# Kernel optimization log

Hardware: AMD Instinct MI355X
Metric: run time of the kernel (lower is better)

The kernel has to match this reference:

```python
import jax, jax.numpy as jnp
import numpy as np

GAMMA = 2.5
K = 4
RHO = 0.085
TAU_CLIP = 5.0
NUM_HEADS = 8


def setup_inputs() -> dict:
    key = jax.random.key(0)
    ks = jax.random.split(key, 4)
    B, T, C = 2, 2048, 512
    x = jax.random.normal(ks[0], (B, T, C), jnp.float32)
    tau = jax.random.uniform(ks[1], (B, T, T), jnp.float32)
    s = 1.0 / np.sqrt(C)
    Wqkv = jax.random.normal(ks[2], (C, 3 * C), jnp.float32) * s
    bqkv = jnp.zeros((3 * C,), jnp.float32)
    Wproj = jax.random.normal(ks[3], (C, C), jnp.float32) * s
    bproj = jnp.zeros((C,), jnp.float32)
    return dict(x=x, tau=tau, Wqkv=Wqkv, bqkv=bqkv, Wproj=Wproj, bproj=bproj)


def reference(x, tau, Wqkv, bqkv, Wproj, bproj):
    B, T, C = x.shape
    H = NUM_HEADS
    D = C // H
    qkv = x @ Wqkv + bqkv                       # [B,T,3C]
    q, k, v = jnp.split(qkv, 3, axis=-1)
    q = q.reshape(B, T, H, D).transpose(0, 2, 1, 3)   # [B,H,T,D]
    k = k.reshape(B, T, H, D).transpose(0, 2, 1, 3)
    v = v.reshape(B, T, H, D).transpose(0, 2, 1, 3)
    scale = D ** -0.5
    logits = jnp.einsum('bhtd,bhsd->bhts', q, k) * scale   # [B,H,T,T]
    pheromone_bias = GAMMA * jnp.log(tau + 1e-8)           # [B,T,T]
    logits = logits + pheromone_bias[:, None]
    # top-K keys per query from tau define the sparse mask (LOCAL_WINDOW=0)
    k_val = min(K, T)
    idx = jax.lax.top_k(tau, k_val)[1]                     # [B,T,K]
    mask = jnp.zeros((B, T, T), bool).at[
        jnp.arange(B)[:, None, None], jnp.arange(T)[None, :, None], idx
    ].set(True)
    logits = jnp.where(mask[:, None], logits, -jnp.inf)
    attn = jax.nn.softmax(logits, axis=-1)                 # [B,H,T,T]
    # EMA pheromone (tau) update, no gradient in original (torch.no_grad)
    signal = attn.mean(axis=1)                             # [B,T,T]
    tau_new = (1.0 - RHO) * tau + signal ** 3
    tau_new = tau_new / (tau_new.sum(axis=-1, keepdims=True) + 1e-8)
    tau_new = jnp.minimum(tau_new, TAU_CLIP)
    tau_new = jax.lax.stop_gradient(tau_new)
    out = jnp.einsum('bhts,bhsd->bthd', attn, v).reshape(B, T, C)
    out = out @ Wproj + bproj
    return out, tau_new
```

## Files before the change

kernel.cpp:

```cpp
#include <hip/hip_runtime.h>
#include <hip/hip_bf16.h>
#include <math.h>

#define BB 2
#define TT 2048
#define CC 512
#define HH 8
#define DD 64
#define KK 4
#define C3 1536
#define MROWS (BB*TT)

#define G1_NT (C3/64)
#define G1_BLOCKS (G1_NT*(MROWS/128))
#define G2_NT (CC/64)
#define G2_BLOCKS (G2_NT*(MROWS/128))

typedef __attribute__((ext_vector_type(8))) short bf16x8;
typedef __attribute__((ext_vector_type(4))) float floatx4;

static __device__ __forceinline__ unsigned short f2bf(float f) {
  unsigned int u = __float_as_uint(f);
  return (unsigned short)((u + 0x7fffu + ((u >> 16) & 1u)) >> 16);
}
static __device__ __forceinline__ float bf2f(unsigned short u) {
  return __uint_as_float(((unsigned int)u) << 16);
}

template<bool BF16OUT>
static __device__ __forceinline__ void gemm_body(
    int bid, int nt,
    const unsigned short* __restrict__ A,
    const unsigned short* __restrict__ Bt,
    const float* __restrict__ bias,
    void* __restrict__ Cout, int N, int K) {
  __shared__ bf16x8 As[128 * 4];
  __shared__ bf16x8 Bs[64 * 4];
  const int tid  = threadIdx.x;
  const int wave = tid >> 6;
  const int lane = tid & 63;
  const int n0 = (bid % nt) * 64;
  const int m0 = (bid / nt) * 128;
  const int m_off = (wave >> 1) * 64;
  const int n_off = (wave & 1) * 32;
  const int lrow = lane >> 2;
  const int lx   = ((lane & 3) ^ ((lane >> 3) & 3)) * 8;
  const int fr = lane & 15;
  const int fq = lane >> 4;
  const int key = (fr >> 1) & 3;

  floatx4 acc[4][2];
#pragma unroll
  for (int i = 0; i < 4; ++i)
#pragma unroll
    for (int j = 0; j < 2; ++j) acc[i][j] = (floatx4){0.f, 0.f, 0.f, 0.f};

  for (int k0 = 0; k0 < K; k0 += 32) {
#pragma unroll
    for (int s = 0; s < 2; ++s) {
      int q = wave * 2 + s;
      const unsigned short* ga = A + (size_t)(m0 + q * 16 + lrow) * K + k0 + lx;
      __builtin_amdgcn_global_load_lds(
          (const __attribute__((address_space(1))) void*)ga,
          (__attribute__((address_space(3))) void*)((char*)As + q * 1024), 16, 0, 0);
    }
    const unsigned short* gb = Bt + (size_t)(n0 + wave * 16 + lrow) * K + k0 + lx;
    __builtin_amdgcn_global_load_lds(
        (const __attribute__((address_space(1))) void*)gb,
        (__attribute__((address_space(3))) void*)((char*)Bs + wave * 1024), 16, 0, 0);
    __syncthreads();
    bf16x8 a[4], b[2];
#pragma unroll
    for (int i = 0; i < 4; ++i)
      a[i] = As[(m_off + i * 16 + fr) * 4 + (fq ^ key)];
#pragma unroll
    for (int j = 0; j < 2; ++j)
      b[j] = Bs[(n_off + j * 16 + fr) * 4 + (fq ^ key)];
#pragma unroll
    for (int i = 0; i < 4; ++i)
#pragma unroll
      for (int j = 0; j < 2; ++j)
        acc[i][j] = __builtin_amdgcn_mfma_f32_16x16x32_bf16(a[i], b[j], acc[i][j], 0, 0, 0);
    __syncthreads();
  }
#pragma unroll
  for (int j = 0; j < 2; ++j) {
    int col = n0 + n_off + j * 16 + fr;
    float bv = bias[col];
#pragma unroll
    for (int i = 0; i < 4; ++i) {
#pragma unroll
      for (int r = 0; r < 4; ++r) {
        int row = m0 + m_off + i * 16 + fq * 4 + r;
        float v = acc[i][j][r] + bv;
        if (BF16OUT) ((unsigned short*)Cout)[(size_t)row * N + col] = f2bf(v);
        else         ((float*)Cout)[(size_t)row * N + col] = v;
      }
    }
  }
}

static __device__ __forceinline__ bool kv_better(float av, int ai, float bv, int bi) {
  return av > bv || (av == bv && ai < bi);
}
static __device__ __forceinline__ void kv_ce(float* v, int* i, int a, int b) {
  if (!kv_better(v[a], i[a], v[b], i[b])) {
    float tv = v[a]; v[a] = v[b]; v[b] = tv;
    int   ti = i[a]; i[a] = i[b]; i[b] = ti;
  }
}
static __device__ __forceinline__ void kv_merge(
    float* av, int* ai, const float* bv, const int* bi) {
  float cv[4]; int ci[4];
#pragma unroll
  for (int j = 0; j < 4; ++j) {
    bool t = kv_better(av[j], ai[j], bv[3 - j], bi[3 - j]);
    cv[j] = t ? av[j] : bv[3 - j];
    ci[j] = t ? ai[j] : bi[3 - j];
  }
  kv_ce(cv, ci, 0, 2); kv_ce(cv, ci, 1, 3);
  kv_ce(cv, ci, 0, 1); kv_ce(cv, ci, 2, 3);
#pragma unroll
  for (int j = 0; j < 4; ++j) { av[j] = cv[j]; ai[j] = ci[j]; }
}

static __device__ __forceinline__ void topk_body(
    int row, const float* __restrict__ tau, int* __restrict__ idx_out) {
  const int tid = threadIdx.x;
  const float4* rp = (const float4*)(tau + (size_t)row * TT);
  float4 f0 = rp[tid * 2], f1 = rp[tid * 2 + 1];
  float e[8] = { f0.x, f0.y, f0.z, f0.w, f1.x, f1.y, f1.z, f1.w };
  const int base = tid * 8;

  float tv[4] = { -1e30f, -1e30f, -1e30f, -1e30f };
  int   ti[4] = { 1 << 30, 1 << 30, 1 << 30, 1 << 30 };
#pragma unroll
  for (int k = 0; k < 8; ++k) {
    float v = e[k];
    if (v > tv[3]) {
      tv[3] = v; ti[3] = base + k;
      if (tv[3] > tv[2]) { float a=tv[2]; tv[2]=tv[3]; tv[3]=a; int b=ti[2]; ti[2]=ti[3]; ti[3]=b; }
      if (tv[2] > tv[1]) { float a=tv[1]; tv[1]=tv[2]; tv[2]=a; int b=ti[1]; ti[1]=ti[2]; ti[2]=b; }
      if (tv[1] > tv[0]) { float a=tv[0]; tv[0]=tv[1]; tv[1]=a; int b=ti[0]; ti[0]=ti[1]; ti[1]=b; }
    }
  }

#pragma unroll
  for (int step = 1; step <= 32; step <<= 1) {
    float bv[4]; int bi[4];
#pragma unroll
    for (int j = 0; j < 4; ++j) {
      bv[j] = __shfl_xor(tv[j], step, 64);
      bi[j] = __shfl_xor(ti[j], step, 64);
    }
    kv_merge(tv, ti, bv, bi);
  }

  __shared__ float swv[4][4];
  __shared__ int   swi[4][4];
  const int wave = tid >> 6, lane = tid & 63;
  if (lane == 0) {
#pragma unroll
    for (int j = 0; j < 4; ++j) { swv[wave][j] = tv[j]; swi[wave][j] = ti[j]; }
  }
  __syncthreads();
  if (tid == 0) {
    float m0[4], m1[4]; int x0[4], x1[4];
#pragma unroll
    for (int j = 0; j < 4; ++j) { m0[j] = swv[0][j]; x0[j] = swi[0][j]; }
#pragma unroll
    for (int j = 0; j < 4; ++j) { m1[j] = swv[1][j]; x1[j] = swi[1][j]; }
    kv_merge(m0, x0, m1, x1);
#pragma unroll
    for (int j = 0; j < 4; ++j) { m1[j] = swv[2][j]; x1[j] = swi[2][j]; }
    float m2[4]; int x2[4];
#pragma unroll
    for (int j = 0; j < 4; ++j) { m2[j] = swv[3][j]; x2[j] = swi[3][j]; }
    kv_merge(m1, x1, m2, x2);
    kv_merge(m0, x0, m1, x1);
    int4 w = { x0[0], x0[1], x0[2], x0[3] };
    *((int4*)(idx_out + row * KK)) = w;
  }
}

static __device__ __forceinline__ void tau_body(
    int row, const float* __restrict__ tau, const int* __restrict__ idx_in,
    const float* __restrict__ sig_in, float* __restrict__ tau_out) {
  const int tid = threadIdx.x;
  int i4[KK]; float s3[KK];
#pragma unroll
  for (int j = 0; j < KK; ++j) {
    i4[j] = idx_in[row * KK + j];
    float s = sig_in[row * KK + j];
    s3[j] = s * s * s;
  }
  const float4* rp = (const float4*)(tau + (size_t)row * TT);
  float v[8];
  float4 f0 = rp[tid * 2], f1 = rp[tid * 2 + 1];
  v[0]=f0.x; v[1]=f0.y; v[2]=f0.z; v[3]=f0.w;
  v[4]=f1.x; v[5]=f1.y; v[6]=f1.z; v[7]=f1.w;
  const float keep = 1.0f - 0.085f;
  const int base = tid * 8;
  float local = 0.f;
#pragma unroll
  for (int i = 0; i < 8; ++i) {
    float t = keep * v[i];
#pragma unroll
    for (int j = 0; j < KK; ++j)
      if (base + i == i4[j]) t += s3[j];
    v[i] = t;
    local += t;
  }
#pragma unroll
  for (int off = 32; off > 0; off >>= 1) local += __shfl_xor(local, off, 64);
  __shared__ float wsum[4];
  __shared__ float tot;
  if ((tid & 63) == 0) wsum[tid >> 6] = local;
  __syncthreads();
  if (tid == 0) tot = wsum[0] + wsum[1] + wsum[2] + wsum[3];
  __syncthreads();
  float inv = 1.f / (tot + 1e-8f);
  float4* op = (float4*)(tau_out + (size_t)row * TT);
  float4 o0 = { fminf(v[0]*inv,5.f), fminf(v[1]*inv,5.f), fminf(v[2]*inv,5.f), fminf(v[3]*inv,5.f) };
  float4 o1 = { fminf(v[4]*inv,5.f), fminf(v[5]*inv,5.f), fminf(v[6]*inv,5.f), fminf(v[7]*inv,5.f) };
  op[tid * 2] = o0;
  op[tid * 2 + 1] = o1;
}

static __device__ __forceinline__ void transpose_body(
    int t, int nbx, const float* __restrict__ W, unsigned short* __restrict__ Wt,
    int R, int Cn) {
  __shared__ unsigned short tile[32][33];
  const int c0 = (t % nbx) * 32, r0 = (t / nbx) * 32;
  const int tx = threadIdx.x & 31, ty = threadIdx.x >> 5;
#pragma unroll
  for (int i = 0; i < 4; ++i) {
    int r = ty + i * 8;
    tile[r][tx] = f2bf(W[(size_t)(r0 + r) * Cn + c0 + tx]);
  }
  __syncthreads();
#pragma unroll
  for (int i = 0; i < 4; ++i) {
    int r = ty + i * 8;
    Wt[(size_t)(c0 + r) * R + r0 + tx] = tile[tx][r];
  }
}

__global__ __launch_bounds__(256) void prep_kernel(
    const float* __restrict__ x, unsigned short* __restrict__ x_bf,
    const float* __restrict__ Wqkv, unsigned short* __restrict__ wqkv_t,
    const float* __restrict__ Wproj, unsigned short* __restrict__ wproj_t) {
  const int bid = blockIdx.x;
  if (bid < 1024) {
    int g = bid * 256 + threadIdx.x;
    const float4* p = (const float4*)x;
    float4 f0 = p[g * 2], f1 = p[g * 2 + 1];
    union { unsigned short u[8]; uint4 v; } pk;
    pk.u[0]=f2bf(f0.x); pk.u[1]=f2bf(f0.y); pk.u[2]=f2bf(f0.z); pk.u[3]=f2bf(f0.w);
    pk.u[4]=f2bf(f1.x); pk.u[5]=f2bf(f1.y); pk.u[6]=f2bf(f1.z); pk.u[7]=f2bf(f1.w);
    ((uint4*)x_bf)[g] = pk.v;
  } else if (bid < 1024 + 768) {
    transpose_body(bid - 1024, C3 / 32, Wqkv, wqkv_t, CC, C3);
  } else {
    transpose_body(bid - 1792, CC / 32, Wproj, wproj_t, CC, CC);
  }
}

__global__ __launch_bounds__(256) void gemm1_topk_kernel(
    const unsigned short* __restrict__ x_bf,
    const unsigned short* __restrict__ wqkv_t,
    const float* __restrict__ bqkv, unsigned short* __restrict__ qkv_bf,
    const float* __restrict__ tau, int* __restrict__ idx_out) {
  if (blockIdx.x < G1_BLOCKS)
    gemm_body<true>(blockIdx.x, G1_NT, x_bf, wqkv_t, bqkv, qkv_bf, C3, CC);
  else
    topk_body(blockIdx.x - G1_BLOCKS, tau, idx_out);
}

__global__ __launch_bounds__(512) void attn_kernel(
    const unsigned short* __restrict__ qkv, const float* __restrict__ tau,
    const int* __restrict__ idx_in, unsigned short* __restrict__ attn_bf,
    float* __restrict__ sig_out) {
  const int row  = blockIdx.x;
  const int b    = row >> 11;
  const int tid  = threadIdx.x;
  const int h    = tid >> 6;
  const int lane = tid & 63;

  __shared__ int   idx4[KK];
  __shared__ float tau4[KK];
  __shared__ float ps[HH][KK];
  if (tid < KK) {
    int s = idx_in[row * KK + tid];
    idx4[tid] = s;
    tau4[tid] = tau[(size_t)row * TT + s];
  }
  __syncthreads();

  const float q = bf2f(qkv[(size_t)row * C3 + h * DD + lane]);
  float kv[KK], vv[KK];
#pragma unroll
  for (int j = 0; j < KK; ++j) {
    size_t bs = ((size_t)(b * TT + idx4[j])) * C3 + h * DD + lane;
    kv[j] = bf2f(qkv[bs + CC]);
    vv[j] = bf2f(qkv[bs + 2 * CC]);
  }

  float p[KK];
#pragma unroll
  for (int j = 0; j < KK; ++j) p[j] = q * kv[j];
#pragma unroll
  for (int off = 32; off > 0; off >>= 1)
#pragma unroll
    for (int j = 0; j < KK; ++j) p[j] += __shfl_xor(p[j], off, 64);

  float logit[KK];
#pragma unroll
  for (int j = 0; j < KK; ++j)
    logit[j] = p[j] * 0.125f + 2.5f * logf(tau4[j] + 1e-8f);

  float m = fmaxf(fmaxf(logit[0], logit[1]), fmaxf(logit[2], logit[3]));
  float den = 0.f;
#pragma unroll
  for (int j = 0; j < KK; ++j) { p[j] = expf(logit[j] - m); den += p[j]; }
  float inv = 1.f / den;
#pragma unroll
  for (int j = 0; j < KK; ++j) p[j] *= inv;

  float o = 0.f;
#pragma unroll
  for (int j = 0; j < KK; ++j) o += p[j] * vv[j];
  attn_bf[(size_t)row * CC + h * DD + lane] = f2bf(o);

  if (lane < KK) ps[h][lane] = p[lane];
  __syncthreads();
  if (tid < KK) {
    float s = 0.f;
#pragma unroll
    for (int k = 0; k < HH; ++k) s += ps[k][tid];
    sig_out[row * KK + tid] = s * (1.0f / HH);
  }
}

__global__ __launch_bounds__(256) void gemm2_tau_kernel(
    const unsigned short* __restrict__ attn_bf,
    const unsigned short* __restrict__ wproj_t,
    const float* __restrict__ bproj, float* __restrict__ out,
    const float* __restrict__ tau, const int* __restrict__ idx_in,
    const float* __restrict__ sig_in, float* __restrict__ tau_out) {
  if (blockIdx.x < G2_BLOCKS)
    gemm_body<false>(blockIdx.x, G2_NT, attn_bf, wproj_t, bproj, out, CC, CC);
  else
    tau_body(blockIdx.x - G2_BLOCKS, tau, idx_in, sig_in, tau_out);
}

extern "C" void kernel_launch(void* const* d_in, const int* in_sizes, int n_in,
                              void* d_out, int out_size, void* d_ws, size_t ws_size,
                              hipStream_t stream) {
  const float* x     = (const float*)d_in[0];
  const float* tau   = (const float*)d_in[1];
  const float* Wqkv  = (const float*)d_in[2];
  const float* bqkv  = (const float*)d_in[3];
  const float* Wproj = (const float*)d_in[4];
  const float* bproj = (const float*)d_in[5];

  float* out     = (float*)d_out;
  float* tau_new = out + (size_t)MROWS * CC;

  char* w = (char*)d_ws;
  unsigned short* qkv_bf  = (unsigned short*)w; w += (size_t)MROWS * C3 * 2;
  unsigned short* x_bf    = (unsigned short*)w; w += (size_t)MROWS * CC * 2;
  unsigned short* wqkv_t  = (unsigned short*)w; w += (size_t)C3 * CC * 2;
  unsigned short* wproj_t = (unsigned short*)w; w += (size_t)CC * CC * 2;
  unsigned short* attn_bf = (unsigned short*)w; w += (size_t)MROWS * CC * 2;
  int*   idx = (int*)w;                  w += (size_t)MROWS * KK * 4;
  float* sig = (float*)w;

  prep_kernel<<<2048, 256, 0, stream>>>(x, x_bf, Wqkv, wqkv_t, Wproj, wproj_t);

  gemm1_topk_kernel<<<G1_BLOCKS + MROWS, 256, 0, stream>>>(
      x_bf, wqkv_t, bqkv, qkv_bf, tau, idx);

  attn_kernel<<<MROWS, 512, 0, stream>>>(qkv_bf, tau, idx, attn_bf, sig);

  gemm2_tau_kernel<<<G2_BLOCKS + MROWS, 256, 0, stream>>>(
      attn_bf, wproj_t, bproj, out, tau, idx, sig, tau_new);
}
```

Measured before the change: 146.3 us.

## Enlarge GEMM tiles to 128x128x64 and add XCD-aware block swizzle

The shared GEMM body moves from 128x64 output tiles with a 32-wide K step to 128x128 tiles with a 64-wide K step. Each wave now computes a 64x64 sub-tile with 16 MFMA accumulators, using a new XOR-swizzled LDS layout. This halves the number of K iterations and barriers and raises operand reuse per LDS load. Block indices are also remapped so that neighbouring tiles land on the same XCD, which should improve L2 sharing. In exchange the grid is half as large, which lowers parallelism for the small projection GEMM, and per-thread register use rises.

New measurement: 151.3 us. 1.03x slower.

```diff
diff --git a/kernel.cpp b/kernel.cpp
--- a/kernel.cpp
+++ b/kernel.cpp
@@ -11,9 +11,9 @@
 #define C3 1536
 #define MROWS (BB*TT)
 
-#define G1_NT (C3/64)
+#define G1_NT (C3/128)
 #define G1_BLOCKS (G1_NT*(MROWS/128))
-#define G2_NT (CC/64)
+#define G2_NT (CC/128)
 #define G2_BLOCKS (G2_NT*(MROWS/128))
 
 typedef __attribute__((ext_vector_type(8))) short bf16x8;
@@ -34,70 +34,81 @@
     const unsigned short* __restrict__ Bt,
     const float* __restrict__ bias,
     void* __restrict__ Cout, int N, int K) {
-  __shared__ bf16x8 As[128 * 4];
-  __shared__ bf16x8 Bs[64 * 4];
+  __shared__ unsigned short As[128][64];
+  __shared__ unsigned short Bs[128][64];
   const int tid  = threadIdx.x;
   const int wave = tid >> 6;
   const int lane = tid & 63;
-  const int n0 = (bid % nt) * 64;
+  const int n0 = (bid % nt) * 128;
   const int m0 = (bid / nt) * 128;
-  const int m_off = (wave >> 1) * 64;
-  const int n_off = (wave & 1) * 32;
-  const int lrow = lane >> 2;
-  const int lx   = ((lane & 3) ^ ((lane >> 3) & 3)) * 8;
+  const int wm = (wave >> 1) * 64;
+  const int wn = (wave & 1) * 64;
   const int fr = lane & 15;
   const int fq = lane >> 4;
-  const int key = (fr >> 1) & 3;
-
-  floatx4 acc[4][2];
+  const int srow   = lane >> 3;
+  const int schunk = ((lane & 7) ^ srow) * 8;
+
+  floatx4 acc[4][4];
 #pragma unroll
   for (int i = 0; i < 4; ++i)
 #pragma unroll
-    for (int j = 0; j < 2; ++j) acc[i][j] = (floatx4){0.f, 0.f, 0.f, 0.f};
-
-  for (int k0 = 0; k0 < K; k0 += 32) {
-#pragma unroll
-    for (int s = 0; s < 2; ++s) {
-      int q = wave * 2 + s;
-      const unsigned short* ga = A + (size_t)(m0 + q * 16 + lrow) * K + k0 + lx;
+    for (int j = 0; j < 4; ++j) acc[i][j] = (floatx4){0.f, 0.f, 0.f, 0.f};
+
+  for (int k0 = 0; k0 < K; k0 += 64) {
+#pragma unroll
+    for (int s = 0; s < 4; ++s) {
+      const int r0 = wave * 32 + s * 8;
+      const unsigned short* ga = A + (size_t)(m0 + r0 + srow) * K + k0 + schunk;
       __builtin_amdgcn_global_load_lds(
           (const __attribute__((address_space(1))) void*)ga,
-          (__attribute__((address_space(3))) void*)((char*)As + q * 1024), 16, 0, 0);
+          (__attribute__((address_space(3))) void*)&As[r0][0], 16, 0, 0);
+      const unsigned short* gb = Bt + (size_t)(n0 + r0 + srow) * K + k0 + schunk;
+      __builtin_amdgcn_global_load_lds(
+          (const __attribute__((address_space(1))) void*)gb,
+          (__attribute__((address_space(3))) void*)&Bs[r0][0], 16, 0, 0);
     }
-    const unsigned short* gb = Bt + (size_t)(n0 + wave * 16 + lrow) * K + k0 + lx;
-    __builtin_amdgcn_global_load_lds(
-        (const __attribute__((address_space(1))) void*)gb,
-        (__attribute__((address_space(3))) void*)((char*)Bs + wave * 1024), 16, 0, 0);
     __syncthreads();
-    bf16x8 a[4], b[2];
-#pragma unroll
-    for (int i = 0; i < 4; ++i)
-      a[i] = As[(m_off + i * 16 + fr) * 4 + (fq ^ key)];
-#pragma unroll
-    for (int j = 0; j < 2; ++j)
-      b[j] = Bs[(n_off + j * 16 + fr) * 4 + (fq ^ key)];
-#pragma unroll
-    for (int i = 0; i < 4; ++i)
-#pragma unroll
-      for (int j = 0; j < 2; ++j)
-        acc[i][j] = __builtin_amdgcn_mfma_f32_16x16x32_bf16(a[i], b[j], acc[i][j], 0, 0, 0);
+#pragma unroll
+    for (int kk = 0; kk < 2; ++kk) {
+      bf16x8 a[4], b[4];
+#pragma unroll
+      for (int i = 0; i < 4; ++i) {
+        const int row = wm + i * 16 + fr;
+        a[i] = *(const bf16x8*)&As[row][(((kk << 2) + fq) ^ (row & 7)) * 8];
+      }
+#pragma unroll
+      for (int j = 0; j < 4; ++j) {
+        const int row = wn + j * 16 + fr;
+        b[j] = *(const bf16x8*)&Bs[row][(((kk << 2) + fq) ^ (row & 7)) * 8];
+      }
+#pragma unroll
+      for (int i = 0; i < 4; ++i)
+#pragma unroll
+        for (int j = 0; j < 4; ++j)
+          acc[i][j] = __builtin_amdgcn_mfma_f32_16x16x32_bf16(a[i], b[j], acc[i][j], 0, 0, 0);
+    }
     __syncthreads();
   }
 #pragma unroll
-  for (int j = 0; j < 2; ++j) {
-    int col = n0 + n_off + j * 16 + fr;
-    float bv = bias[col];
+  for (int j = 0; j < 4; ++j) {
+    const int col = n0 + wn + j * 16 + fr;
+    const float bv = bias[col];
 #pragma unroll
     for (int i = 0; i < 4; ++i) {
 #pragma unroll
       for (int r = 0; r < 4; ++r) {
-        int row = m0 + m_off + i * 16 + fq * 4 + r;
-        float v = acc[i][j][r] + bv;
+        const int row = m0 + wm + i * 16 + fq * 4 + r;
+        const float v = acc[i][j][r] + bv;
         if (BF16OUT) ((unsigned short*)Cout)[(size_t)row * N + col] = f2bf(v);
         else         ((float*)Cout)[(size_t)row * N + col] = v;
       }
     }
   }
+}
+
+static __device__ __forceinline__ int xcd_swz(int bid, int nblk) {
+  const int cpx = nblk >> 3;
+  return (bid & 7) * cpx + (bid >> 3);
 }
 
 static __device__ __forceinline__ bool kv_better(float av, int ai, float bv, int bi) {
@@ -272,7 +283,8 @@
     const float* __restrict__ bqkv, unsigned short* __restrict__ qkv_bf,
     const float* __restrict__ tau, int* __restrict__ idx_out) {
   if (blockIdx.x < G1_BLOCKS)
-    gemm_body<true>(blockIdx.x, G1_NT, x_bf, wqkv_t, bqkv, qkv_bf, C3, CC);
+    gemm_body<true>(xcd_swz(blockIdx.x, G1_BLOCKS), G1_NT,
+                    x_bf, wqkv_t, bqkv, qkv_bf, C3, CC);
   else
     topk_body(blockIdx.x - G1_BLOCKS, tau, idx_out);
 }
@@ -349,7 +361,8 @@
     const float* __restrict__ tau, const int* __restrict__ idx_in,
     const float* __restrict__ sig_in, float* __restrict__ tau_out) {
   if (blockIdx.x < G2_BLOCKS)
-    gemm_body<false>(blockIdx.x, G2_NT, attn_bf, wproj_t, bproj, out, CC, CC);
+    gemm_body<false>(xcd_swz(blockIdx.x, G2_BLOCKS), G2_NT,
+                     attn_bf, wproj_t, bproj, out, CC, CC);
   else
     tau_body(blockIdx.x - G2_BLOCKS, tau, idx_in, sig_in, tau_out);
 }
```
